# Performance work log

Hardware: AMD Instinct MI355X
Metric: run time of the kernel (lower is better)

Reference implementation:

```python
import jax, jax.numpy as jnp
import numpy as np

B, S, D, H = 2, 2048, 1024, 16
DH = D // H              # 64
BLK = S // 16            # 128, default block_size = seq_len // 16
NB = S // BLK            # 16 blocks per axis


def setup_inputs() -> dict:
    key = jax.random.key(0)
    ks = jax.random.split(key, 7)
    scale = 0.02
    x = jax.random.normal(ks[0], (B, S, D), jnp.float32)
    Wq = jax.random.normal(ks[1], (D, D), jnp.float32) * scale
    Wk = jax.random.normal(ks[2], (D, D), jnp.float32) * scale
    Wv = jax.random.normal(ks[3], (D, D), jnp.float32) * scale
    Wo = jax.random.normal(ks[4], (D, D), jnp.float32) * scale
    bo = jnp.zeros((D,), jnp.float32)
    # keep-block decisions: torch.rand(1) > sparsity(=0.5) per (i,j) block
    block_mask = jax.random.randint(ks[5], (NB, NB), 0, 2).astype(bool)
    # keep diagonal blocks so no query row is fully masked (avoids NaN softmax)
    block_mask = block_mask | jnp.eye(NB, dtype=bool)
    return {"x": x, "Wq": Wq, "Wk": Wk, "Wv": Wv, "Wo": Wo, "bo": bo,
            "block_mask": block_mask}


def reference(x, Wq, Wk, Wv, Wo, bo, block_mask):
    # projections (torch Linear: y = x @ W.T), split heads -> [B,H,S,DH]
    def split(t):
        return t.reshape(B, S, H, DH).transpose(0, 2, 1, 3)
    q = split(x @ Wq.T)
    k = split(x @ Wk.T)
    v = split(x @ Wv.T)

    scores = jnp.einsum('bhqd,bhkd->bhqk', q, k) / jnp.sqrt(jnp.float32(DH))
    # expand [NB,NB] block mask to [S,S]; shared across batch and heads
    mask_full = jnp.repeat(jnp.repeat(block_mask, BLK, axis=0), BLK, axis=1)
    scores = jnp.where(mask_full, scores, -jnp.inf)
    attn = jax.nn.softmax(scores, axis=-1)        # dropout = identity (eval)
    out = jnp.einsum('bhqk,bhkd->bhqd', attn, v)
    out = out.transpose(0, 2, 1, 3).reshape(B, S, D)
    return out @ Wo.T + bo
```

## Files before the change

### kernel.cpp

```cpp
#include <hip/hip_runtime.h>
#include <hip/hip_bf16.h>


typedef __attribute__((ext_vector_type(4))) float f32x4;
typedef __attribute__((ext_vector_type(8))) short bf16x8;

#define MFMA16(a, b, c) __builtin_amdgcn_mfma_f32_16x16x32_bf16(a, b, c, 0, 0, 0)
#define LOG2E 1.4426950408889634f

__device__ inline unsigned short f2bf(float f) {
  unsigned u = __builtin_bit_cast(unsigned, f);
  unsigned rounding = 0x7FFFu + ((u >> 16) & 1u);
  return (unsigned short)((u + rounding) >> 16);
}

__global__ __launch_bounds__(256) void cvt_kernel(const float* __restrict__ in,
                                                  unsigned short* __restrict__ out, int n8) {
  const int i = blockIdx.x * 256 + threadIdx.x;
  if (i >= n8) return;
  const float4* p = (const float4*)in + (size_t)i * 2;
  const float4 a = p[0], b = p[1];
  union { unsigned short u[8]; uint4 v; } r;
  r.u[0] = f2bf(a.x); r.u[1] = f2bf(a.y); r.u[2] = f2bf(a.z); r.u[3] = f2bf(a.w);
  r.u[4] = f2bf(b.x); r.u[5] = f2bf(b.y); r.u[6] = f2bf(b.z); r.u[7] = f2bf(b.w);
  *((uint4*)out + i) = r.v;
}

__device__ inline int mask_mode(const void* maskp) {
  const unsigned short* mh = (const unsigned short*)maskp;
  const unsigned* mw = (const unsigned*)maskp;
  bool anyFloatHalf = false;
  for (int t = 0; t < 128; ++t) {
    const unsigned short v = mh[t];
    if (v == 0x3F80u || v == 0x3C00u) { anyFloatHalf = true; break; }
  }
  if (anyFloatHalf) {
    bool evenNZ = false;
    for (int t = 0; t < 128; t += 2)
      if (mh[t] != 0) { evenNZ = true; break; }
    return evenNZ ? 1 : 0;
  }
  bool anyBig = false;
  for (int t = 0; t < 64; ++t)
    if (mw[t] > 1u) { anyBig = true; break; }
  if (anyBig) return 2;
  bool oddNZ = false;
  for (int t = 1; t < 64; t += 2)
    if (mw[t] != 0u) { oddNZ = true; break; }
  return oddNZ ? 3 : 4;
}

__device__ inline int mask_read(const void* maskp, int mode, int idx) {
  switch (mode) {
    case 0: return ((const unsigned*)maskp)[idx] != 0u;
    case 1: return ((const unsigned short*)maskp)[idx] != 0;
    case 2: return ((const unsigned char*)maskp)[idx] != 0;
    case 3: return ((const int*)maskp)[idx] != 0;
    default: return ((const unsigned*)maskp)[idx * 2] != 0u ||
                    ((const unsigned*)maskp)[idx * 2 + 1] != 0u;
  }
}

__device__ inline void stage_tile_128x32(const __hip_bfloat16* g, int ld_elems,
                                         __hip_bfloat16* lds, int wave, int lane) {
#pragma unroll
  for (int i = 0; i < 2; ++i) {
    const int chunk = wave * 2 + i;
    const int o = chunk * 1024 + lane * 16;
    const int r = o >> 6;
    const int cb = o & 63;
    const char* ga = (const char*)g + (size_t)r * ld_elems * 2 + cb;
    __builtin_amdgcn_global_load_lds(
        (const __attribute__((address_space(1))) unsigned int*)ga,
        (__attribute__((address_space(3))) unsigned int*)((char*)lds + chunk * 1024),
        16, 0, 0);
  }
}

template <int MODE>
__global__ __launch_bounds__(256) void gemm_bt(
    const __hip_bfloat16* __restrict__ A,
    const __hip_bfloat16* __restrict__ W0, const __hip_bfloat16* __restrict__ W1,
    const float* __restrict__ bias,
    __hip_bfloat16* __restrict__ OutB, float* __restrict__ OutF, int K) {
  __shared__ __hip_bfloat16 sA[128 * 32];
  __shared__ __hip_bfloat16 sB[128 * 32];
  const int tid = threadIdx.x;
  const int wave = tid >> 6, lane = tid & 63;
  const int lr = lane & 15, lg = lane >> 4;
  const int wr = wave >> 1, wc = wave & 1;
  const int m0 = blockIdx.x * 128;

  const __hip_bfloat16* W;
  __hip_bfloat16* OB = nullptr;
  int n0;
  if (MODE == 0) {
    const int sel = blockIdx.y >> 3;
    n0 = (blockIdx.y & 7) * 128;
    W = sel ? W1 : W0;
    OB = OutB + (size_t)sel * 4194304ull;
  } else {
    n0 = blockIdx.y * 128;
    W = W0;
    OB = OutB;
  }

  f32x4 acc[4][4] = {};
  for (int k0 = 0; k0 < K; k0 += 32) {
    stage_tile_128x32(A + (size_t)m0 * K + k0, K, sA, wave, lane);
    stage_tile_128x32(W + (size_t)n0 * K + k0, K, sB, wave, lane);
    __syncthreads();

    bf16x8 af[4], bfr[4];
#pragma unroll
    for (int mi = 0; mi < 4; ++mi)
      af[mi] = *(const bf16x8*)(sA + (64 * wr + 16 * mi + lr) * 32 + lg * 8);
#pragma unroll
    for (int ni = 0; ni < 4; ++ni)
      bfr[ni] = *(const bf16x8*)(sB + (64 * wc + 16 * ni + lr) * 32 + lg * 8);
#pragma unroll
    for (int i = 0; i < 4; ++i)
#pragma unroll
      for (int jj = 0; jj < 4; ++jj)
        acc[i][jj] = (MODE == 2) ? MFMA16(bfr[i], af[jj], acc[i][jj])
                                 : MFMA16(af[i], bfr[jj], acc[i][jj]);
    __syncthreads();
  }

  if (MODE == 2) {
#pragma unroll
    for (int i = 0; i < 4; ++i)
#pragma unroll
      for (int jj = 0; jj < 4; ++jj)
#pragma unroll
        for (int q = 0; q < 4; ++q) {
          const int n = n0 + 64 * wc + 16 * i + lg * 4 + q;
          const int m = m0 + 64 * wr + 16 * jj + lr;
          OB[((size_t)(m >> 11) * 1024 + n) * 2048 + (m & 2047)] =
              __float2bfloat16(acc[i][jj][q]);
        }
  } else {
#pragma unroll
    for (int i = 0; i < 4; ++i)
#pragma unroll
      for (int jj = 0; jj < 4; ++jj)
#pragma unroll
        for (int q = 0; q < 4; ++q) {
          const int m = m0 + 64 * wr + 16 * i + lg * 4 + q;
          const int n = n0 + 64 * wc + 16 * jj + lr;
          if (MODE == 0) OB[(size_t)m * 1024 + n] = __float2bfloat16(acc[i][jj][q]);
          else           OutF[(size_t)m * 1024 + n] = acc[i][jj][q] + bias[n];
        }
  }
}

__global__ __launch_bounds__(256) void attn_kernel(
    const __hip_bfloat16* __restrict__ Q, const __hip_bfloat16* __restrict__ K,
    const __hip_bfloat16* __restrict__ Vt, const void* __restrict__ maskp,
    __hip_bfloat16* __restrict__ O) {
  __shared__ char uK[128 * 128];
  __shared__ char sV[64 * 256];
  __shared__ __hip_bfloat16 P_lds[4][16][136];

  const int qc = blockIdx.x, bh = blockIdx.y;
  const int b = bh >> 4, h = bh & 15;
  const int tid = threadIdx.x, wave = tid >> 6, lane = tid & 63;
  const int lr = lane & 15, lg = lane >> 4;

  const int mmode = mask_mode(maskp);
  const int qb = qc >> 1;
  int keep[16], nkeep = 0;
  for (int j = 0; j < 16; ++j)
    if (mask_read(maskp, mmode, qb * 16 + j)) keep[nkeep++] = j;

  const size_t base = (size_t)b * 2048 * 1024 + (size_t)h * 64;
  const char* Kbase  = (const char*)(K + base);
  const char* Vtbase = (const char*)Vt +
      ((size_t)b * 1024 * 2048 + (size_t)h * 64 * 2048) * 2;
  const int qrow0 = qc * 64 + wave * 16;

  bf16x8 qf[2];
#pragma unroll
  for (int ks = 0; ks < 2; ++ks)
    qf[ks] = *(const bf16x8*)(Q + base + (size_t)(qrow0 + lr) * 1024 + ks * 32 + lg * 8);

  f32x4 oa[4] = {};
  float mrun[4], lrun[4];
#pragma unroll
  for (int q = 0; q < 4; ++q) { mrun[q] = -1e30f; lrun[q] = 0.f; }

  for (int ji = 0; ji < nkeep; ++ji) {
    const int j = keep[ji];
    const char* gK = Kbase + (size_t)j * 128 * 2048;
    const char* gV = Vtbase + (size_t)j * 128 * 2;

#pragma unroll
    for (int i = 0; i < 4; ++i) {
      const int o = (wave * 4 + i) * 1024 + lane * 16;
      { const int r = o >> 7, cb = o & 127, cbs = cb ^ ((r & 7) << 4);
        __builtin_amdgcn_global_load_lds(
            (const __attribute__((address_space(1))) unsigned*)(gK + (size_t)r * 2048 + cbs),
            (__attribute__((address_space(3))) unsigned*)(uK + o), 16, 0, 0); }
      { const int r = o >> 8, cb = o & 255, cbs = cb ^ ((r & 7) << 4);
        __builtin_amdgcn_global_load_lds(
            (const __attribute__((address_space(1))) unsigned*)(gV + (size_t)r * 4096 + cbs),
            (__attribute__((address_space(3))) unsigned*)(sV + o), 16, 0, 0); }
    }
    __syncthreads();

    f32x4 s[8] = {};
    __builtin_amdgcn_s_setprio(1);
#pragma unroll
    for (int ks = 0; ks < 2; ++ks)
#pragma unroll
      for (int nt = 0; nt < 8; ++nt) {
        const int row = 16 * nt + lr;
        bf16x8 kf = *(const bf16x8*)(uK + row * 128 + ((ks * 64 + lg * 16) ^ ((lr & 7) << 4)));
        s[nt] = MFMA16(qf[ks], kf, s[nt]);
      }
    __builtin_amdgcn_s_setprio(0);

#pragma unroll
    for (int q = 0; q < 4; ++q) {
      float rm = -1e30f;
#pragma unroll
      for (int nt = 0; nt < 8; ++nt) {
        s[nt][q] *= 0.125f;
        rm = fmaxf(rm, s[nt][q]);
      }
      rm = fmaxf(rm, __shfl_xor(rm, 1));
      rm = fmaxf(rm, __shfl_xor(rm, 2));
      rm = fmaxf(rm, __shfl_xor(rm, 4));
      rm = fmaxf(rm, __shfl_xor(rm, 8));
      const float mold = mrun[q];
      const float mnew = fmaxf(mold, rm);
      const float sf = exp2f((mold - mnew) * LOG2E);
      float rs = 0.f;
#pragma unroll
      for (int nt = 0; nt < 8; ++nt) {
        const float p = exp2f((s[nt][q] - mnew) * LOG2E);
        s[nt][q] = p;
        rs += p;
      }
      rs += __shfl_xor(rs, 1);
      rs += __shfl_xor(rs, 2);
      rs += __shfl_xor(rs, 4);
      rs += __shfl_xor(rs, 8);
      lrun[q] = lrun[q] * sf + rs;
      mrun[q] = mnew;
#pragma unroll
      for (int ni = 0; ni < 4; ++ni) oa[ni][q] *= sf;
    }

#pragma unroll
    for (int nt = 0; nt < 8; ++nt)
#pragma unroll
      for (int q = 0; q < 4; ++q)
        P_lds[wave][lg * 4 + q][16 * nt + lr] = __float2bfloat16(s[nt][q]);

    __builtin_amdgcn_s_setprio(1);
#pragma unroll
    for (int ks = 0; ks < 4; ++ks) {
      bf16x8 pa = *(const bf16x8*)&P_lds[wave][lr][ks * 32 + lg * 8];
#pragma unroll
      for (int ni = 0; ni < 4; ++ni) {
        const int row = 16 * ni + lr;
        bf16x8 vb = *(const bf16x8*)(sV + row * 256 + ((ks * 64 + lg * 16) ^ ((lr & 7) << 4)));
        oa[ni] = MFMA16(pa, vb, oa[ni]);
      }
    }
    __builtin_amdgcn_s_setprio(0);
    __syncthreads();
  }

#pragma unroll
  for (int ni = 0; ni < 4; ++ni)
#pragma unroll
    for (int q = 0; q < 4; ++q) {
      const int row = qrow0 + lg * 4 + q;
      const float v = oa[ni][q] / fmaxf(lrun[q], 1e-30f);
      O[base + (size_t)row * 1024 + 16 * ni + lr] = __float2bfloat16(v);
    }
}

extern "C" void kernel_launch(void* const* d_in, const int* in_sizes, int n_in,
                              void* d_out, int out_size, void* d_ws, size_t ws_size,
                              hipStream_t stream) {
  const float* x  = (const float*)d_in[0];
  const float* Wq = (const float*)d_in[1];
  const float* Wk = (const float*)d_in[2];
  const float* Wv = (const float*)d_in[3];
  const float* Wo = (const float*)d_in[4];
  const float* bo = (const float*)d_in[5];
  const void* mask = d_in[6];
  float* out = (float*)d_out;

  __hip_bfloat16* ws = (__hip_bfloat16*)d_ws;
  __hip_bfloat16* xb  = ws;
  __hip_bfloat16* Wqb = ws + 4194304ull;
  __hip_bfloat16* Wkb = ws + 5242880ull;
  __hip_bfloat16* Wvb = ws + 6291456ull;
  __hip_bfloat16* Wob = ws + 7340032ull;
  __hip_bfloat16* Qb  = ws + 8388608ull;
  __hip_bfloat16* Kb  = ws + 12582912ull;
  __hip_bfloat16* Vtb = ws + 16777216ull;
  __hip_bfloat16* Ob  = ws + 20971520ull;

  dim3 blk(256);
  cvt_kernel<<<2048, blk, 0, stream>>>(x,  (unsigned short*)xb,  524288);
  cvt_kernel<<<512,  blk, 0, stream>>>(Wq, (unsigned short*)Wqb, 131072);
  cvt_kernel<<<512,  blk, 0, stream>>>(Wk, (unsigned short*)Wkb, 131072);
  cvt_kernel<<<512,  blk, 0, stream>>>(Wv, (unsigned short*)Wvb, 131072);
  cvt_kernel<<<512,  blk, 0, stream>>>(Wo, (unsigned short*)Wob, 131072);
  gemm_bt<0><<<dim3(32, 16), blk, 0, stream>>>(xb, Wqb, Wkb, nullptr, Qb, nullptr, 1024);
  gemm_bt<2><<<dim3(32, 8), blk, 0, stream>>>(xb, Wvb, nullptr, nullptr, Vtb, nullptr, 1024);
  attn_kernel<<<dim3(32, 32), blk, 0, stream>>>(Qb, Kb, Vtb, mask, Ob);
  gemm_bt<1><<<dim3(32, 8), blk, 0, stream>>>(Ob, Wob, nullptr, bo, nullptr, out, 1024);
}
```

Measured before the change: 300.1 us.

## Merge conversion and QKV launches; read K/V directly from global in attention

Folds the five fp32-to-bf16 conversion launches into one kernel and the Q/K and V projection GEMMs into one launch with a 24-wide grid, cutting launch count and tail effects. The attention kernel no longer stages K and V tiles through LDS with barriers. Each wave now loads its MFMA operands straight from global memory, and the kernel gets a higher occupancy hint. This removes the LDS round-trip and the synchronisation, but each wave repeats the global/L2 loads, and the V reads are strided.

```diff
diff --git a/kernel.cpp b/kernel.cpp
--- a/kernel.cpp
+++ b/kernel.cpp
@@ -14,16 +14,25 @@
   return (unsigned short)((u + rounding) >> 16);
 }
 
-__global__ __launch_bounds__(256) void cvt_kernel(const float* __restrict__ in,
-                                                  unsigned short* __restrict__ out, int n8) {
+__global__ __launch_bounds__(256) void cvt_all(
+    const float* __restrict__ x, const float* __restrict__ wq,
+    const float* __restrict__ wk, const float* __restrict__ wv,
+    const float* __restrict__ wo, unsigned short* __restrict__ dst) {
   const int i = blockIdx.x * 256 + threadIdx.x;
-  if (i >= n8) return;
-  const float4* p = (const float4*)in + (size_t)i * 2;
+  if (i >= 1048576) return;
+  const float* src;
+  size_t off;
+  if (i < 524288)      { src = x;  off = i; }
+  else if (i < 655360) { src = wq; off = i - 524288; }
+  else if (i < 786432) { src = wk; off = i - 655360; }
+  else if (i < 917504) { src = wv; off = i - 786432; }
+  else                 { src = wo; off = i - 917504; }
+  const float4* p = (const float4*)src + off * 2;
   const float4 a = p[0], b = p[1];
   union { unsigned short u[8]; uint4 v; } r;
   r.u[0] = f2bf(a.x); r.u[1] = f2bf(a.y); r.u[2] = f2bf(a.z); r.u[3] = f2bf(a.w);
   r.u[4] = f2bf(b.x); r.u[5] = f2bf(b.y); r.u[6] = f2bf(b.z); r.u[7] = f2bf(b.w);
-  *((uint4*)out + i) = r.v;
+  *((uint4*)dst + i) = r.v;
 }
 
 __device__ inline int mask_mode(const void* maskp) {
@@ -77,12 +86,11 @@
   }
 }
 
-template <int MODE>
-__global__ __launch_bounds__(256) void gemm_bt(
+__global__ __launch_bounds__(256) void gemm_qkv(
     const __hip_bfloat16* __restrict__ A,
-    const __hip_bfloat16* __restrict__ W0, const __hip_bfloat16* __restrict__ W1,
-    const float* __restrict__ bias,
-    __hip_bfloat16* __restrict__ OutB, float* __restrict__ OutF, int K) {
+    const __hip_bfloat16* __restrict__ Wq, const __hip_bfloat16* __restrict__ Wk,
+    const __hip_bfloat16* __restrict__ Wv,
+    __hip_bfloat16* __restrict__ QK, __hip_bfloat16* __restrict__ Vt) {
   __shared__ __hip_bfloat16 sA[128 * 32];
   __shared__ __hip_bfloat16 sB[128 * 32];
   const int tid = threadIdx.x;
@@ -90,25 +98,14 @@
   const int lr = lane & 15, lg = lane >> 4;
   const int wr = wave >> 1, wc = wave & 1;
   const int m0 = blockIdx.x * 128;
-
-  const __hip_bfloat16* W;
-  __hip_bfloat16* OB = nullptr;
-  int n0;
-  if (MODE == 0) {
-    const int sel = blockIdx.y >> 3;
-    n0 = (blockIdx.y & 7) * 128;
-    W = sel ? W1 : W0;
-    OB = OutB + (size_t)sel * 4194304ull;
-  } else {
-    n0 = blockIdx.y * 128;
-    W = W0;
-    OB = OutB;
-  }
+  const int sel = blockIdx.y >> 3;
+  const int n0 = (blockIdx.y & 7) * 128;
+  const __hip_bfloat16* W = (sel == 0) ? Wq : ((sel == 1) ? Wk : Wv);
 
   f32x4 acc[4][4] = {};
-  for (int k0 = 0; k0 < K; k0 += 32) {
-    stage_tile_128x32(A + (size_t)m0 * K + k0, K, sA, wave, lane);
-    stage_tile_128x32(W + (size_t)n0 * K + k0, K, sB, wave, lane);
+  for (int k0 = 0; k0 < 1024; k0 += 32) {
+    stage_tile_128x32(A + (size_t)m0 * 1024 + k0, 1024, sA, wave, lane);
+    stage_tile_128x32(W + (size_t)n0 * 1024 + k0, 1024, sB, wave, lane);
     __syncthreads();
 
     bf16x8 af[4], bfr[4];
@@ -118,16 +115,35 @@
 #pragma unroll
     for (int ni = 0; ni < 4; ++ni)
       bfr[ni] = *(const bf16x8*)(sB + (64 * wc + 16 * ni + lr) * 32 + lg * 8);
+    if (sel < 2) {
+#pragma unroll
+      for (int i = 0; i < 4; ++i)
+#pragma unroll
+        for (int jj = 0; jj < 4; ++jj)
+          acc[i][jj] = MFMA16(af[i], bfr[jj], acc[i][jj]);
+    } else {
+#pragma unroll
+      for (int i = 0; i < 4; ++i)
+#pragma unroll
+        for (int jj = 0; jj < 4; ++jj)
+          acc[i][jj] = MFMA16(bfr[i], af[jj], acc[i][jj]);
+    }
+    __syncthreads();
+  }
+
+  if (sel < 2) {
+    __hip_bfloat16* OB = QK + (size_t)sel * 4194304ull;
 #pragma unroll
     for (int i = 0; i < 4; ++i)
 #pragma unroll
       for (int jj = 0; jj < 4; ++jj)
-        acc[i][jj] = (MODE == 2) ? MFMA16(bfr[i], af[jj], acc[i][jj])
-                                 : MFMA16(af[i], bfr[jj], acc[i][jj]);
-    __syncthreads();
-  }
-
-  if (MODE == 2) {
+#pragma unroll
+        for (int q = 0; q < 4; ++q) {
+          const int m = m0 + 64 * wr + 16 * i + lg * 4 + q;
+          const int n = n0 + 64 * wc + 16 * jj + lr;
+          OB[(size_t)m * 1024 + n] = __float2bfloat16(acc[i][jj][q]);
+        }
+  } else {
 #pragma unroll
     for (int i = 0; i < 4; ++i)
 #pragma unroll
@@ -136,30 +152,61 @@
         for (int q = 0; q < 4; ++q) {
           const int n = n0 + 64 * wc + 16 * i + lg * 4 + q;
           const int m = m0 + 64 * wr + 16 * jj + lr;
-          OB[((size_t)(m >> 11) * 1024 + n) * 2048 + (m & 2047)] =
+          Vt[((size_t)(m >> 11) * 1024 + n) * 2048 + (m & 2047)] =
               __float2bfloat16(acc[i][jj][q]);
         }
-  } else {
+  }
+}
+
+__global__ __launch_bounds__(256) void gemm_out(
+    const __hip_bfloat16* __restrict__ A, const __hip_bfloat16* __restrict__ W,
+    const float* __restrict__ bias, float* __restrict__ OutF) {
+  __shared__ __hip_bfloat16 sA[128 * 32];
+  __shared__ __hip_bfloat16 sB[128 * 32];
+  const int tid = threadIdx.x;
+  const int wave = tid >> 6, lane = tid & 63;
+  const int lr = lane & 15, lg = lane >> 4;
+  const int wr = wave >> 1, wc = wave & 1;
+  const int m0 = blockIdx.x * 128;
+  const int n0 = blockIdx.y * 128;
+
+  f32x4 acc[4][4] = {};
+  for (int k0 = 0; k0 < 1024; k0 += 32) {
+    stage_tile_128x32(A + (size_t)m0 * 1024 + k0, 1024, sA, wave, lane);
+    stage_tile_128x32(W + (size_t)n0 * 1024 + k0, 1024, sB, wave, lane);
+    __syncthreads();
+
+    bf16x8 af[4], bfr[4];
+#pragma unroll
+    for (int mi = 0; mi < 4; ++mi)
+      af[mi] = *(const bf16x8*)(sA + (64 * wr + 16 * mi + lr) * 32 + lg * 8);
+#pragma unroll
+    for (int ni = 0; ni < 4; ++ni)
+      bfr[ni] = *(const bf16x8*)(sB + (64 * wc + 16 * ni + lr) * 32 + lg * 8);
 #pragma unroll
     for (int i = 0; i < 4; ++i)
 #pragma unroll
       for (int jj = 0; jj < 4; ++jj)
-#pragma unroll
-        for (int q = 0; q < 4; ++q) {
-          const int m = m0 + 64 * wr + 16 * i + lg * 4 + q;
-          const int n = n0 + 64 * wc + 16 * jj + lr;
-          if (MODE == 0) OB[(size_t)m * 1024 + n] = __float2bfloat16(acc[i][jj][q]);
-          else           OutF[(size_t)m * 1024 + n] = acc[i][jj][q] + bias[n];
-        }
-  }
-}
-
-__global__ __launch_bounds__(256) void attn_kernel(
+        acc[i][jj] = MFMA16(af[i], bfr[jj], acc[i][jj]);
+    __syncthreads();
+  }
+
+#pragma unroll
+  for (int i = 0; i < 4; ++i)
+#pragma unroll
+    for (int jj = 0; jj < 4; ++jj)
+#pragma unroll
+      for (int q = 0; q < 4; ++q) {
+        const int m = m0 + 64 * wr + 16 * i + lg * 4 + q;
+        const int n = n0 + 64 * wc + 16 * jj + lr;
+        OutF[(size_t)m * 1024 + n] = acc[i][jj][q] + bias[n];
+      }
+}
+
+__global__ __launch_bounds__(256, 4) void attn_kernel(
     const __hip_bfloat16* __restrict__ Q, const __hip_bfloat16* __restrict__ K,
     const __hip_bfloat16* __restrict__ Vt, const void* __restrict__ maskp,
     __hip_bfloat16* __restrict__ O) {
-  __shared__ char uK[128 * 128];
-  __shared__ char sV[64 * 256];
   __shared__ __hip_bfloat16 P_lds[4][16][136];
 
   const int qc = blockIdx.x, bh = blockIdx.y;
@@ -174,7 +221,7 @@
     if (mask_read(maskp, mmode, qb * 16 + j)) keep[nkeep++] = j;
 
   const size_t base = (size_t)b * 2048 * 1024 + (size_t)h * 64;
-  const char* Kbase  = (const char*)(K + base);
+  const char* Kbase = (const char*)(K + base);
   const char* Vtbase = (const char*)Vt +
       ((size_t)b * 1024 * 2048 + (size_t)h * 64 * 2048) * 2;
   const int qrow0 = qc * 64 + wave * 16;
@@ -194,28 +241,13 @@
     const char* gK = Kbase + (size_t)j * 128 * 2048;
     const char* gV = Vtbase + (size_t)j * 128 * 2;
 
-#pragma unroll
-    for (int i = 0; i < 4; ++i) {
-      const int o = (wave * 4 + i) * 1024 + lane * 16;
-      { const int r = o >> 7, cb = o & 127, cbs = cb ^ ((r & 7) << 4);
-        __builtin_amdgcn_global_load_lds(
-            (const __attribute__((address_space(1))) unsigned*)(gK + (size_t)r * 2048 + cbs),
-            (__attribute__((address_space(3))) unsigned*)(uK + o), 16, 0, 0); }
-      { const int r = o >> 8, cb = o & 255, cbs = cb ^ ((r & 7) << 4);
-        __builtin_amdgcn_global_load_lds(
-            (const __attribute__((address_space(1))) unsigned*)(gV + (size_t)r * 4096 + cbs),
-            (__attribute__((address_space(3))) unsigned*)(sV + o), 16, 0, 0); }
-    }
-    __syncthreads();
-
     f32x4 s[8] = {};
     __builtin_amdgcn_s_setprio(1);
 #pragma unroll
     for (int ks = 0; ks < 2; ++ks)
 #pragma unroll
       for (int nt = 0; nt < 8; ++nt) {
-        const int row = 16 * nt + lr;
-        bf16x8 kf = *(const bf16x8*)(uK + row * 128 + ((ks * 64 + lg * 16) ^ ((lr & 7) << 4)));
+        bf16x8 kf = *(const bf16x8*)(gK + (size_t)(16 * nt + lr) * 2048 + (ks * 32 + lg * 8) * 2);
         s[nt] = MFMA16(qf[ks], kf, s[nt]);
       }
     __builtin_amdgcn_s_setprio(0);
@@ -264,13 +296,11 @@
       bf16x8 pa = *(const bf16x8*)&P_lds[wave][lr][ks * 32 + lg * 8];
 #pragma unroll
       for (int ni = 0; ni < 4; ++ni) {
-        const int row = 16 * ni + lr;
-        bf16x8 vb = *(const bf16x8*)(sV + row * 256 + ((ks * 64 + lg * 16) ^ ((lr & 7) << 4)));
+        bf16x8 vb = *(const bf16x8*)(gV + (size_t)(16 * ni + lr) * 4096 + (ks * 32 + lg * 8) * 2);
         oa[ni] = MFMA16(pa, vb, oa[ni]);
       }
     }
     __builtin_amdgcn_s_setprio(0);
-    __syncthreads();
   }
 
 #pragma unroll
@@ -302,18 +332,12 @@
   __hip_bfloat16* Wvb = ws + 6291456ull;
   __hip_bfloat16* Wob = ws + 7340032ull;
   __hip_bfloat16* Qb  = ws + 8388608ull;
-  __hip_bfloat16* Kb  = ws + 12582912ull;
   __hip_bfloat16* Vtb = ws + 16777216ull;
   __hip_bfloat16* Ob  = ws + 20971520ull;
 
   dim3 blk(256);
-  cvt_kernel<<<2048, blk, 0, stream>>>(x,  (unsigned short*)xb,  524288);
-  cvt_kernel<<<512,  blk, 0, stream>>>(Wq, (unsigned short*)Wqb, 131072);
-  cvt_kernel<<<512,  blk, 0, stream>>>(Wk, (unsigned short*)Wkb, 131072);
-  cvt_kernel<<<512,  blk, 0, stream>>>(Wv, (unsigned short*)Wvb, 131072);
-  cvt_kernel<<<512,  blk, 0, stream>>>(Wo, (unsigned short*)Wob, 131072);
-  gemm_bt<0><<<dim3(32, 16), blk, 0, stream>>>(xb, Wqb, Wkb, nullptr, Qb, nullptr, 1024);
-  gemm_bt<2><<<dim3(32, 8), blk, 0, stream>>>(xb, Wvb, nullptr, nullptr, Vtb, nullptr, 1024);
-  attn_kernel<<<dim3(32, 32), blk, 0, stream>>>(Qb, Kb, Vtb, mask, Ob);
-  gemm_bt<1><<<dim3(32, 8), blk, 0, stream>>>(Ob, Wob, nullptr, bo, nullptr, out, 1024);
-}
+  cvt_all<<<4096, blk, 0, stream>>>(x, Wq, Wk, Wv, Wo, (unsigned short*)xb);
+  gemm_qkv<<<dim3(32, 24), blk, 0, stream>>>(xb, Wqb, Wkb, Wvb, Qb, Vtb);
+  attn_kernel<<<dim3(32, 32), blk, 0, stream>>>(Qb, Qb + 4194304ull, Vtb, mask, Ob);
+  gemm_out<<<dim3(32, 8), blk, 0, stream>>>(Ob, Wob, bo, out);
+}
```

After: 369.4 us. 23.1% more time.
